# Optimization experiments

Hardware: AMD Instinct MI355X
Metric: run time of the kernel (lower is better)

The kernel has to match this reference:

```python
import jax, jax.numpy as jnp
import numpy as np

K = 7        # kernel_size
OUT = 10     # out_channels
CIN = 1      # in_channels
IH = 306     # input spatial size (square)
POOL = 10    # max_pool1d kernel/stride


def setup_inputs() -> dict:
    key = jax.random.key(0)
    k1, k2, k3 = jax.random.split(key, 3)
    stdv = 1.0 / np.sqrt(CIN * K * K)  # matches reset_parameters()
    x = jax.random.normal(k1, (1, CIN, IH, IH), dtype=jnp.float32)
    K_hit = jax.random.uniform(k2, (OUT, CIN, K, K), dtype=jnp.float32, minval=-stdv, maxval=stdv)
    K_miss = jax.random.uniform(k3, (OUT, CIN, K, K), dtype=jnp.float32, minval=-stdv, maxval=stdv)
    return {"input": x, "K_hit": K_hit, "K_miss": K_miss}


def _patches(x, k):
    # Sliding windows, stride 1, valid padding: (B, C, k, k, fh, fw).
    B, C, H, W = x.shape
    fh, fw = H - k + 1, W - k + 1
    rows = []
    for u in range(k):          # fixed small loop over kernel rows
        cols = [x[:, :, u:u + fh, v:v + fw] for v in range(k)]
        rows.append(jnp.stack(cols, axis=2))   # (B, C, k, fh, fw)
    return jnp.stack(rows, axis=2)             # (B, C, k, k, fh, fw)


def reference(input, K_hit, K_miss):
    B, cin, ih, _ = input.shape
    out, k = K_hit.shape[0], K_hit.shape[2]
    fh = ih - k + 1
    out_fmap = cin * out

    p = _patches(input, k)                                # (B, cin, k, k, fh, fh)
    p = p[:, None]                                        # (B, 1, cin, k, k, fh, fh)
    kh = K_hit[None, :, :, :, :, None, None]              # (1, out, cin, k, k, 1, 1)
    km = K_miss[None, :, :, :, :, None, None]

    # -relu(-(x - K_hit)) == min(x - K_hit, 0); summed over ALL windows + kernel taps -> (B, out)
    F_hit_sum = jnp.sum(jnp.minimum(p - kh, 0.0), axis=(2, 3, 4, 5, 6))
    F_miss_sum = jnp.sum(jnp.maximum(p - km, 0.0), axis=(2, 3, 4, 5, 6))
    F_map_val = F_hit_sum - F_miss_sum                    # (B, out)

    def expand(v):  # broadcast (B, out) scalar-per-channel over (cin*fh*fh), view as feature map
        return jnp.broadcast_to(v[:, :, None], (B, out, cin * fh * fh)).reshape(B, out_fmap, fh, fh)

    F_map = expand(F_map_val)
    F_hit_list = expand(F_hit_sum)
    F_miss_list = expand(F_miss_sum)

    # torch.squeeze then F.max_pool1d(kernel=10): pool over the last spatial axis.
    sq = jnp.squeeze(F_map)                               # (out_fmap, fh, fh) since B=1
    L = sq.shape[-1]
    nwin = L // POOL
    pooled = sq[..., : nwin * POOL].reshape(sq.shape[:-1] + (nwin, POOL)).max(-1)

    return pooled, F_hit_list, F_miss_list
```

## Files before the change

### kernel.cpp

```cpp
#include <hip/hip_runtime.h>

#define IHH 306
#define KW 7
#define OUTC 10
#define FH 300
#define NPIX (FH * FH)
#define KK (KW * KW)
#define BLK 256
#define NBLK_A ((NPIX + BLK - 1) / BLK)
#define NACC (2 * OUTC)
#define OUT_TOTAL 1890000
#define POOLED_END 90000
#define HIT_END 990000

__global__ __launch_bounds__(BLK) void compute_partials(
    const float* __restrict__ x,
    const float* __restrict__ kh,
    const float* __restrict__ km,
    float* __restrict__ partials)
{
    __shared__ float s_kh[OUTC * KK];
    __shared__ float s_km[OUTC * KK];
    for (int t = threadIdx.x; t < OUTC * KK; t += BLK) {
        s_kh[t] = kh[t];
        s_km[t] = km[t];
    }
    __syncthreads();

    float acc_h[OUTC];
    float acc_m[OUTC];
#pragma unroll
    for (int o = 0; o < OUTC; ++o) { acc_h[o] = 0.0f; acc_m[o] = 0.0f; }

    const int p = blockIdx.x * BLK + threadIdx.x;
    if (p < NPIX) {
        const int i = p / FH;
        const int j = p - i * FH;
        const float* xr = x + i * IHH + j;
        for (int u = 0; u < KW; ++u) {
#pragma unroll
            for (int v = 0; v < KW; ++v) {
                const float xv = xr[u * IHH + v];
                const int uv = u * KW + v;
#pragma unroll
                for (int o = 0; o < OUTC; ++o) {
                    const float dh = xv - s_kh[o * KK + uv];
                    const float dm = xv - s_km[o * KK + uv];
                    acc_h[o] += fminf(dh, 0.0f);
                    acc_m[o] += fmaxf(dm, 0.0f);
                }
            }
        }
    }

    const int lane = threadIdx.x & 63;
    const int wave = threadIdx.x >> 6;
    __shared__ float s_red[BLK / 64][NACC];
#pragma unroll
    for (int o = 0; o < OUTC; ++o) {
        float h = acc_h[o];
        float m = acc_m[o];
#pragma unroll
        for (int s = 32; s > 0; s >>= 1) {
            h += __shfl_xor(h, s);
            m += __shfl_xor(m, s);
        }
        if (lane == 0) {
            s_red[wave][o] = h;
            s_red[wave][OUTC + o] = m;
        }
    }
    __syncthreads();
    if (threadIdx.x < NACC) {
        float s = s_red[0][threadIdx.x] + s_red[1][threadIdx.x]
                + s_red[2][threadIdx.x] + s_red[3][threadIdx.x];
        partials[blockIdx.x * NACC + threadIdx.x] = s;
    }
}

__global__ void reduce_finals(const float* __restrict__ partials,
                              float* __restrict__ finals)
{
    const int a = threadIdx.x;
    if (a < NACC) {
        float s = 0.0f;
        for (int b = 0; b < NBLK_A; ++b) s += partials[b * NACC + a];
        finals[a] = s;
    }
}

__global__ __launch_bounds__(BLK) void fill_out(
    const float* __restrict__ finals,
    float4* __restrict__ out)
{
    const int idx4 = blockIdx.x * BLK + threadIdx.x;
    if (idx4 >= OUT_TOTAL / 4) return;
    const int base = idx4 * 4;
    float val;
    if (base < POOLED_END) {
        const int o = base / 9000;
        val = finals[o] - finals[OUTC + o];
    } else if (base < HIT_END) {
        const int o = (base - POOLED_END) / 90000;
        val = finals[o];
    } else {
        const int o = (base - HIT_END) / 90000;
        val = finals[OUTC + o];
    }
    out[idx4] = make_float4(val, val, val, val);
}

extern "C" void kernel_launch(void* const* d_in, const int* in_sizes, int n_in,
                              void* d_out, int out_size, void* d_ws, size_t ws_size,
                              hipStream_t stream) {
    const float* x  = (const float*)d_in[0];
    const float* kh = (const float*)d_in[1];
    const float* km = (const float*)d_in[2];
    float* out = (float*)d_out;

    float* partials = (float*)d_ws;
    float* finals   = partials + NBLK_A * NACC;

    compute_partials<<<NBLK_A, BLK, 0, stream>>>(x, kh, km, partials);
    reduce_finals<<<1, 64, 0, stream>>>(partials, finals);

    const int n4 = OUT_TOTAL / 4;
    fill_out<<<(n4 + BLK - 1) / BLK, BLK, 0, stream>>>(finals, (float4*)out);
}
```

Measured before the change: 31.47 us.

## Use abs-difference identity for min/max sums and fuse final reduction into fill

Rewrites min(d,0) and max(d,0) as (d-|d|)/2 and (d+|d|)/2, so the inner loop only accumulates |x-k| per channel. The linear part comes from a global sum of x and per-channel kernel sums. Kernel weights are interleaved as float2 in shared memory. The separate single-block reduce kernel is removed: every fill block now redundantly reduces the transposed partials itself, saving one launch but repeating that reduction in each block and risking float cancellation in the large linear terms.

```diff
diff --git a/kernel.cpp b/kernel.cpp
--- a/kernel.cpp
+++ b/kernel.cpp
@@ -7,30 +7,32 @@
 #define NPIX (FH * FH)
 #define KK (KW * KW)
 #define BLK 256
-#define NBLK_A ((NPIX + BLK - 1) / BLK)
-#define NACC (2 * OUTC)
+#define NBA ((NPIX + BLK - 1) / BLK)
+#define NROWS 21
 #define OUT_TOTAL 1890000
 #define POOLED_END 90000
 #define HIT_END 990000
 
-__global__ __launch_bounds__(BLK) void compute_partials(
+
+__global__ __launch_bounds__(BLK) void k_partials(
     const float* __restrict__ x,
     const float* __restrict__ kh,
     const float* __restrict__ km,
-    float* __restrict__ partials)
+    float* __restrict__ partials,
+    float* __restrict__ ksums)
 {
-    __shared__ float s_kh[OUTC * KK];
-    __shared__ float s_km[OUTC * KK];
-    for (int t = threadIdx.x; t < OUTC * KK; t += BLK) {
-        s_kh[t] = kh[t];
-        s_km[t] = km[t];
+    __shared__ float2 s_k[KK * OUTC];
+    for (int t = threadIdx.x; t < KK * OUTC; t += BLK) {
+        const int tap = t / OUTC;
+        const int o = t - tap * OUTC;
+        s_k[t] = make_float2(kh[o * KK + tap], km[o * KK + tap]);
     }
     __syncthreads();
 
-    float acc_h[OUTC];
-    float acc_m[OUTC];
+    float ah[OUTC], am[OUTC];
+    float sx = 0.0f;
 #pragma unroll
-    for (int o = 0; o < OUTC; ++o) { acc_h[o] = 0.0f; acc_m[o] = 0.0f; }
+    for (int o = 0; o < OUTC; ++o) { ah[o] = 0.0f; am[o] = 0.0f; }
 
     const int p = blockIdx.x * BLK + threadIdx.x;
     if (p < NPIX) {
@@ -38,16 +40,15 @@
         const int j = p - i * FH;
         const float* xr = x + i * IHH + j;
         for (int u = 0; u < KW; ++u) {
-#pragma unroll
             for (int v = 0; v < KW; ++v) {
                 const float xv = xr[u * IHH + v];
-                const int uv = u * KW + v;
+                sx += xv;
+                const float2* wk = &s_k[(u * KW + v) * OUTC];
 #pragma unroll
                 for (int o = 0; o < OUTC; ++o) {
-                    const float dh = xv - s_kh[o * KK + uv];
-                    const float dm = xv - s_km[o * KK + uv];
-                    acc_h[o] += fminf(dh, 0.0f);
-                    acc_m[o] += fmaxf(dm, 0.0f);
+                    const float2 w = wk[o];
+                    ah[o] += fabsf(xv - w.x);
+                    am[o] += fabsf(xv - w.y);
                 }
             }
         }
@@ -55,57 +56,84 @@
 
     const int lane = threadIdx.x & 63;
     const int wave = threadIdx.x >> 6;
-    __shared__ float s_red[BLK / 64][NACC];
+    __shared__ float s_red[BLK / 64][NROWS];
+
+    float vals[NROWS];
 #pragma unroll
-    for (int o = 0; o < OUTC; ++o) {
-        float h = acc_h[o];
-        float m = acc_m[o];
+    for (int o = 0; o < OUTC; ++o) { vals[o] = ah[o]; vals[OUTC + o] = am[o]; }
+    vals[2 * OUTC] = sx;
+
 #pragma unroll
-        for (int s = 32; s > 0; s >>= 1) {
-            h += __shfl_xor(h, s);
-            m += __shfl_xor(m, s);
-        }
-        if (lane == 0) {
-            s_red[wave][o] = h;
-            s_red[wave][OUTC + o] = m;
-        }
+    for (int r = 0; r < NROWS; ++r) {
+        float v = vals[r];
+#pragma unroll
+        for (int s = 32; s > 0; s >>= 1) v += __shfl_xor(v, s);
+        if (lane == 0) s_red[wave][r] = v;
     }
     __syncthreads();
-    if (threadIdx.x < NACC) {
-        float s = s_red[0][threadIdx.x] + s_red[1][threadIdx.x]
-                + s_red[2][threadIdx.x] + s_red[3][threadIdx.x];
-        partials[blockIdx.x * NACC + threadIdx.x] = s;
+    if (threadIdx.x < NROWS) {
+        const float s = s_red[0][threadIdx.x] + s_red[1][threadIdx.x]
+                      + s_red[2][threadIdx.x] + s_red[3][threadIdx.x];
+        partials[threadIdx.x * NBA + blockIdx.x] = s;
+    }
+
+    if (blockIdx.x == 0 && threadIdx.x < 2 * OUTC) {
+        const float* kp = (threadIdx.x < OUTC)
+            ? (kh + threadIdx.x * KK)
+            : (km + (threadIdx.x - OUTC) * KK);
+        float s = 0.0f;
+        for (int t = 0; t < KK; ++t) s += kp[t];
+        ksums[threadIdx.x] = s;
     }
 }
 
-__global__ void reduce_finals(const float* __restrict__ partials,
-                              float* __restrict__ finals)
-{
-    const int a = threadIdx.x;
-    if (a < NACC) {
-        float s = 0.0f;
-        for (int b = 0; b < NBLK_A; ++b) s += partials[b * NACC + a];
-        finals[a] = s;
-    }
-}
-
-__global__ __launch_bounds__(BLK) void fill_out(
-    const float* __restrict__ finals,
+__global__ __launch_bounds__(BLK) void k_fill(
+    const float* __restrict__ partials,
+    const float* __restrict__ ksums,
     float4* __restrict__ out)
 {
-    const int idx4 = blockIdx.x * BLK + threadIdx.x;
+    __shared__ float s_part[NROWS][8];
+    __shared__ float s_o[3][OUTC];
+    const int t = threadIdx.x;
+
+    if (t < NROWS * 8) {
+        const int r = t >> 3;
+        const int s = t & 7;
+        const float* row = partials + r * NBA;
+        float acc = 0.0f;
+        for (int c = s; c < NBA; c += 8) acc += row[c];
+        s_part[r][s] = acc;
+    }
+    __syncthreads();
+    if (t < NROWS) {
+        float f = 0.0f;
+#pragma unroll
+        for (int s = 0; s < 8; ++s) f += s_part[t][s];
+        s_part[t][0] = f;
+    }
+    __syncthreads();
+    if (t < OUTC) {
+        const float Sx = s_part[2 * OUTC][0];
+        const float Ah = s_part[t][0];
+        const float Am = s_part[OUTC + t][0];
+        const float Fh = 0.5f * ((Sx - (float)NPIX * ksums[t]) - Ah);
+        const float Fm = 0.5f * ((Sx - (float)NPIX * ksums[OUTC + t]) + Am);
+        s_o[0][t] = Fh - Fm;
+        s_o[1][t] = Fh;
+        s_o[2][t] = Fm;
+    }
+    __syncthreads();
+
+    const int idx4 = blockIdx.x * BLK + t;
     if (idx4 >= OUT_TOTAL / 4) return;
     const int base = idx4 * 4;
     float val;
     if (base < POOLED_END) {
-        const int o = base / 9000;
-        val = finals[o] - finals[OUTC + o];
+        val = s_o[0][base / 9000];
     } else if (base < HIT_END) {
-        const int o = (base - POOLED_END) / 90000;
-        val = finals[o];
+        val = s_o[1][(base - POOLED_END) / 90000];
     } else {
-        const int o = (base - HIT_END) / 90000;
-        val = finals[OUTC + o];
+        val = s_o[2][(base - HIT_END) / 90000];
     }
     out[idx4] = make_float4(val, val, val, val);
 }
@@ -119,11 +147,10 @@
     float* out = (float*)d_out;
 
     float* partials = (float*)d_ws;
-    float* finals   = partials + NBLK_A * NACC;
+    float* ksums    = partials + NROWS * NBA;
 
-    compute_partials<<<NBLK_A, BLK, 0, stream>>>(x, kh, km, partials);
-    reduce_finals<<<1, 64, 0, stream>>>(partials, finals);
+    k_partials<<<NBA, BLK, 0, stream>>>(x, kh, km, partials, ksums);
 
     const int n4 = OUT_TOTAL / 4;
-    fill_out<<<(n4 + BLK - 1) / BLK, BLK, 0, stream>>>(finals, (float4*)out);
+    k_fill<<<(n4 + BLK - 1) / BLK, BLK, 0, stream>>>(partials, ksums, (float4*)out);
 }
```

Result: no change. 30.86 us (-1.9%).
